# Performance work log

Hardware: AMD Instinct MI355X
Metric: run time of the kernel (lower is better)

Reference implementation:

```python
import jax, jax.numpy as jnp
import numpy as np


def setup_inputs() -> dict:
    key = jax.random.key(0)
    k1, k2, k3, k4, k5 = jax.random.split(key, 5)
    B, T, D = 4, 4096, 2048
    Dr = D // 4  # low-rank projection dim (512)
    s = 1.0 / np.sqrt(D)  # torch Linear default init scale
    return {
        "hidden": jax.random.normal(k1, (B, T, D), dtype=jnp.float32),
        "Wq": jax.random.normal(k2, (Dr, D), dtype=jnp.float32) * s,
        "bq": jax.random.normal(k3, (Dr,), dtype=jnp.float32) * s,
        "Wk": jax.random.normal(k4, (Dr, D), dtype=jnp.float32) * s,
        "bk": jax.random.normal(k5, (Dr,), dtype=jnp.float32) * s,
    }


def reference(hidden, Wq, bq, Wk, bk):
    # hidden: (B, T, D); torch Linear is x @ W.T + b with W: (Dr, D)
    q = jnp.einsum("btd,rd->btr", hidden, Wq) + bq  # (B, T, Dr)
    k = jnp.einsum("btd,rd->btr", hidden, Wk) + bk  # (B, T, Dr)
    scale = q.shape[-1] ** -0.5
    # Faithful to source: full (B, T, T) attention logits, then mean over keys
    attn = jnp.einsum("btr,bsr->bts", q, k) * scale  # (B, T, T)
    scores = attn.mean(axis=-1)  # (B, T)
    return scores
```

## Files before the change

kernel.cpp:

```cpp
#include <hip/hip_runtime.h>


constexpr int B  = 4;
constexpr int T  = 4096;
constexpr int D  = 2048;
constexpr int DR = 512;

constexpr int NZ  = 128;
constexpr int NRC = 4;

__global__ __launch_bounds__(256)
void colsum_part_k(const float* __restrict__ hidden, float* __restrict__ part) {
    const int d4 = blockIdx.x * 256 + threadIdx.x;
    const int b  = blockIdx.y;
    const int z  = blockIdx.z;
    const int rows = T / NZ;
    const int t0 = z * rows;
    const float4* src = reinterpret_cast<const float4*>(hidden + (size_t)b * T * D);
    float4 acc = make_float4(0.f, 0.f, 0.f, 0.f);
#pragma unroll 8
    for (int t = t0; t < t0 + rows; ++t) {
        float4 v = src[(size_t)t * (D / 4) + d4];
        acc.x += v.x; acc.y += v.y; acc.z += v.z; acc.w += v.w;
    }
    float4* dst = reinterpret_cast<float4*>(part + ((size_t)z * B + b) * D);
    dst[d4] = acc;
}

__global__ __launch_bounds__(256)
void hsum_reduce_k(const float* __restrict__ part, float* __restrict__ hsum) {
    const int d = blockIdx.x * 256 + threadIdx.x;
    const int b = blockIdx.y;
    float acc = 0.f;
#pragma unroll 8
    for (int z = 0; z < NZ; ++z) acc += part[((size_t)z * B + b) * D + d];
    hsum[(size_t)b * D + d] = acc;
}

__global__ __launch_bounds__(256)
void kbar_k(const float* __restrict__ Wk, const float* __restrict__ bk,
            const float* __restrict__ hsum, float* __restrict__ kbar) {
    const int b    = blockIdx.y;
    const int wave = threadIdx.x >> 6;
    const int lane = threadIdx.x & 63;
    const int r    = blockIdx.x * 4 + wave;
    const float4* wrow = reinterpret_cast<const float4*>(Wk + (size_t)r * D);
    const float4* h    = reinterpret_cast<const float4*>(hsum + (size_t)b * D);
    float acc = 0.f;
#pragma unroll
    for (int i = 0; i < D / 4 / 64; ++i) {
        const int idx = i * 64 + lane;
        float4 wv = wrow[idx];
        float4 hv = h[idx];
        acc += wv.x * hv.x + wv.y * hv.y + wv.z * hv.z + wv.w * hv.w;
    }
#pragma unroll
    for (int off = 32; off; off >>= 1) acc += __shfl_down(acc, off);
    if (lane == 0) kbar[b * DR + r] = acc * (1.0f / T) + bk[r];
}

__global__ __launch_bounds__(256)
void wqpart_k(const float* __restrict__ Wq, const float* __restrict__ kbar,
              float* __restrict__ wqpart) {
    const int d  = blockIdx.x * 256 + threadIdx.x;
    const int b  = blockIdx.y;
    const int c  = blockIdx.z;
    const int r0 = c * (DR / NRC);
    const float* kb = kbar + b * DR;
    float acc = 0.f;
#pragma unroll 8
    for (int r = r0; r < r0 + DR / NRC; ++r)
        acc += Wq[(size_t)r * D + d] * kb[r];
    wqpart[((size_t)c * B + b) * D + d] = acc;
}

__global__ __launch_bounds__(256)
void finish_k(const float* __restrict__ wqpart, const float* __restrict__ bq,
              const float* __restrict__ kbar, float* __restrict__ wqeff,
              float* __restrict__ cterm) {
    __shared__ float wsum[4];
    const int d = blockIdx.x * 256 + threadIdx.x;
    const int b = blockIdx.y;
    float acc = 0.f;
#pragma unroll
    for (int c = 0; c < NRC; ++c) acc += wqpart[((size_t)c * B + b) * D + d];
    wqeff[(size_t)b * D + d] = acc;

    if (blockIdx.x == 0) {
        const float* kb = kbar + b * DR;
        const int tid = threadIdx.x;
        float a2 = bq[tid] * kb[tid] + bq[tid + 256] * kb[tid + 256];
#pragma unroll
        for (int off = 32; off; off >>= 1) a2 += __shfl_down(a2, off);
        if ((tid & 63) == 0) wsum[tid >> 6] = a2;
        __syncthreads();
        if (tid == 0) cterm[b] = wsum[0] + wsum[1] + wsum[2] + wsum[3];
    }
}

__global__ __launch_bounds__(256)
void scores_k(const float* __restrict__ hidden, const float* __restrict__ wqeff,
              const float* __restrict__ cterm, float* __restrict__ out) {
    const int b    = blockIdx.y;
    const int wave = threadIdx.x >> 6;
    const int lane = threadIdx.x & 63;
    const int t    = blockIdx.x * 4 + wave;
    const float4* hrow = reinterpret_cast<const float4*>(hidden + ((size_t)b * T + t) * D);
    const float4* w    = reinterpret_cast<const float4*>(wqeff + (size_t)b * D);
    float acc = 0.f;
#pragma unroll
    for (int i = 0; i < D / 4 / 64; ++i) {
        const int idx = i * 64 + lane;
        float4 hv = hrow[idx];
        float4 wv = w[idx];
        acc += hv.x * wv.x + hv.y * wv.y + hv.z * wv.z + hv.w * wv.w;
    }
#pragma unroll
    for (int off = 32; off; off >>= 1) acc += __shfl_down(acc, off);
    if (lane == 0) out[(size_t)b * T + t] = (acc + cterm[b]) * 4.41941738241592e-02f;
}

extern "C" void kernel_launch(void* const* d_in, const int* in_sizes, int n_in,
                              void* d_out, int out_size, void* d_ws, size_t ws_size,
                              hipStream_t stream) {
    const float* hidden = (const float*)d_in[0];
    const float* Wq     = (const float*)d_in[1];
    const float* bq     = (const float*)d_in[2];
    const float* Wk     = (const float*)d_in[3];
    const float* bk     = (const float*)d_in[4];
    float* out = (float*)d_out;

    float* part   = (float*)d_ws;
    float* hsum   = part + (size_t)NZ * B * D;
    float* kbar   = hsum + B * D;
    float* wqpart = kbar + B * DR;
    float* wqeff  = wqpart + (size_t)NRC * B * D;
    float* cterm  = wqeff + B * D;

    dim3 g1(D / 1024, B, NZ);
    colsum_part_k<<<g1, 256, 0, stream>>>(hidden, part);

    dim3 g1b(D / 256, B);
    hsum_reduce_k<<<g1b, 256, 0, stream>>>(part, hsum);

    dim3 g2(DR / 4, B);
    kbar_k<<<g2, 256, 0, stream>>>(Wk, bk, hsum, kbar);

    dim3 g3(D / 256, B, NRC);
    wqpart_k<<<g3, 256, 0, stream>>>(Wq, kbar, wqpart);

    dim3 g4(D / 256, B);
    finish_k<<<g4, 256, 0, stream>>>(wqpart, bq, kbar, wqeff, cterm);

    dim3 g5(T / 4, B);
    scores_k<<<g5, 256, 0, stream>>>(hidden, wqeff, cterm, out);
}
```

Measured before the change: 244.1 us.

## Fuse partial-sum reduction into kbar and drop split-r Wq partial pass

Merges the column-sum reduction with the Wk projection into one kernel that keeps each batch's summed hidden vector in shared memory. It also replaces the split-over-r Wq partial products plus finish kernel with a single kernel that loops over all 512 ranks, staging kbar in shared memory. Together these cut the launch chain from six kernels to four and remove intermediate global round-trips. The cost is much lower parallelism in the middle stages: 32 blocks for the reduce/kbar step (each redoing the partial-sum reduction) and 32 blocks for the Wq pass.

Result: slower. 341.8 us (+40.0%).

```diff
diff --git a/kernel.cpp b/kernel.cpp
--- a/kernel.cpp
+++ b/kernel.cpp
@@ -5,9 +5,7 @@
 constexpr int T  = 4096;
 constexpr int D  = 2048;
 constexpr int DR = 512;
-
-constexpr int NZ  = 128;
-constexpr int NRC = 4;
+constexpr int NZ = 128;
 
 __global__ __launch_bounds__(256)
 void colsum_part_k(const float* __restrict__ hidden, float* __restrict__ part) {
@@ -23,72 +21,63 @@
         float4 v = src[(size_t)t * (D / 4) + d4];
         acc.x += v.x; acc.y += v.y; acc.z += v.z; acc.w += v.w;
     }
-    float4* dst = reinterpret_cast<float4*>(part + ((size_t)z * B + b) * D);
-    dst[d4] = acc;
+    reinterpret_cast<float4*>(part + ((size_t)z * B + b) * D)[d4] = acc;
 }
 
 __global__ __launch_bounds__(256)
-void hsum_reduce_k(const float* __restrict__ part, float* __restrict__ hsum) {
-    const int d = blockIdx.x * 256 + threadIdx.x;
-    const int b = blockIdx.y;
-    float acc = 0.f;
+void redkbar_k(const float* __restrict__ part, const float* __restrict__ Wk,
+               const float* __restrict__ bk, float* __restrict__ kbar) {
+    __shared__ float hs[D];
+    const int b   = blockIdx.y;
+    const int rc  = blockIdx.x;
+    const int tid = threadIdx.x;
+#pragma unroll
+    for (int j = 0; j < D / 256; ++j) {
+        const int d = j * 256 + tid;
+        float acc = 0.f;
 #pragma unroll 8
-    for (int z = 0; z < NZ; ++z) acc += part[((size_t)z * B + b) * D + d];
-    hsum[(size_t)b * D + d] = acc;
+        for (int z = 0; z < NZ; ++z) acc += part[((size_t)z * B + b) * D + d];
+        hs[d] = acc;
+    }
+    __syncthreads();
+    const int wave = tid >> 6, lane = tid & 63;
+    const float4* hs4 = reinterpret_cast<const float4*>(hs);
+    for (int j = 0; j < 16; ++j) {
+        const int r = rc * 64 + wave * 16 + j;
+        const float4* wrow = reinterpret_cast<const float4*>(Wk + (size_t)r * D);
+        float acc = 0.f;
+#pragma unroll
+        for (int i = 0; i < D / 4 / 64; ++i) {
+            const int idx = i * 64 + lane;
+            float4 wv = wrow[idx];
+            float4 hv = hs4[idx];
+            acc += wv.x * hv.x + wv.y * hv.y + wv.z * hv.z + wv.w * hv.w;
+        }
+#pragma unroll
+        for (int off = 32; off; off >>= 1) acc += __shfl_down(acc, off);
+        if (lane == 0) kbar[b * DR + r] = acc * (1.0f / T) + bk[r];
+    }
 }
 
 __global__ __launch_bounds__(256)
-void kbar_k(const float* __restrict__ Wk, const float* __restrict__ bk,
-            const float* __restrict__ hsum, float* __restrict__ kbar) {
-    const int b    = blockIdx.y;
-    const int wave = threadIdx.x >> 6;
-    const int lane = threadIdx.x & 63;
-    const int r    = blockIdx.x * 4 + wave;
-    const float4* wrow = reinterpret_cast<const float4*>(Wk + (size_t)r * D);
-    const float4* h    = reinterpret_cast<const float4*>(hsum + (size_t)b * D);
-    float acc = 0.f;
-#pragma unroll
-    for (int i = 0; i < D / 4 / 64; ++i) {
-        const int idx = i * 64 + lane;
-        float4 wv = wrow[idx];
-        float4 hv = h[idx];
-        acc += wv.x * hv.x + wv.y * hv.y + wv.z * hv.z + wv.w * hv.w;
-    }
-#pragma unroll
-    for (int off = 32; off; off >>= 1) acc += __shfl_down(acc, off);
-    if (lane == 0) kbar[b * DR + r] = acc * (1.0f / T) + bk[r];
-}
-
-__global__ __launch_bounds__(256)
-void wqpart_k(const float* __restrict__ Wq, const float* __restrict__ kbar,
-              float* __restrict__ wqpart) {
-    const int d  = blockIdx.x * 256 + threadIdx.x;
-    const int b  = blockIdx.y;
-    const int c  = blockIdx.z;
-    const int r0 = c * (DR / NRC);
-    const float* kb = kbar + b * DR;
+void wqeff_k(const float* __restrict__ Wq, const float* __restrict__ bq,
+             const float* __restrict__ kbar, float* __restrict__ wqeff,
+             float* __restrict__ cterm) {
+    __shared__ float kb[DR];
+    __shared__ float wsum[4];
+    const int b   = blockIdx.y;
+    const int tid = threadIdx.x;
+    kb[tid]       = kbar[b * DR + tid];
+    kb[tid + 256] = kbar[b * DR + tid + 256];
+    __syncthreads();
+    const int d = blockIdx.x * 256 + tid;
     float acc = 0.f;
 #pragma unroll 8
-    for (int r = r0; r < r0 + DR / NRC; ++r)
+    for (int r = 0; r < DR; ++r)
         acc += Wq[(size_t)r * D + d] * kb[r];
-    wqpart[((size_t)c * B + b) * D + d] = acc;
-}
-
-__global__ __launch_bounds__(256)
-void finish_k(const float* __restrict__ wqpart, const float* __restrict__ bq,
-              const float* __restrict__ kbar, float* __restrict__ wqeff,
-              float* __restrict__ cterm) {
-    __shared__ float wsum[4];
-    const int d = blockIdx.x * 256 + threadIdx.x;
-    const int b = blockIdx.y;
-    float acc = 0.f;
-#pragma unroll
-    for (int c = 0; c < NRC; ++c) acc += wqpart[((size_t)c * B + b) * D + d];
     wqeff[(size_t)b * D + d] = acc;
 
     if (blockIdx.x == 0) {
-        const float* kb = kbar + b * DR;
-        const int tid = threadIdx.x;
         float a2 = bq[tid] * kb[tid] + bq[tid + 256] * kb[tid + 256];
 #pragma unroll
         for (int off = 32; off; off >>= 1) a2 += __shfl_down(a2, off);
@@ -130,27 +119,19 @@
     const float* bk     = (const float*)d_in[4];
     float* out = (float*)d_out;
 
-    float* part   = (float*)d_ws;
-    float* hsum   = part + (size_t)NZ * B * D;
-    float* kbar   = hsum + B * D;
-    float* wqpart = kbar + B * DR;
-    float* wqeff  = wqpart + (size_t)NRC * B * D;
-    float* cterm  = wqeff + B * D;
+    float* part  = (float*)d_ws;
+    float* kbar  = part + (size_t)NZ * B * D;
+    float* wqeff = kbar + B * DR;
+    float* cterm = wqeff + B * D;
 
     dim3 g1(D / 1024, B, NZ);
     colsum_part_k<<<g1, 256, 0, stream>>>(hidden, part);
 
-    dim3 g1b(D / 256, B);
-    hsum_reduce_k<<<g1b, 256, 0, stream>>>(part, hsum);
+    dim3 g2(8, B);
+    redkbar_k<<<g2, 256, 0, stream>>>(part, Wk, bk, kbar);
 
-    dim3 g2(DR / 4, B);
-    kbar_k<<<g2, 256, 0, stream>>>(Wk, bk, hsum, kbar);
-
-    dim3 g3(D / 256, B, NRC);
-    wqpart_k<<<g3, 256, 0, stream>>>(Wq, kbar, wqpart);
-
-    dim3 g4(D / 256, B);
-    finish_k<<<g4, 256, 0, stream>>>(wqpart, bq, kbar, wqeff, cterm);
+    dim3 g3(D / 256, B);
+    wqeff_k<<<g3, 256, 0, stream>>>(Wq, bq, kbar, wqeff, cterm);
 
     dim3 g5(T / 4, B);
     scores_k<<<g5, 256, 0, stream>>>(hidden, wqeff, cterm, out);
```
